# Performance work log

Measured on AMD Instinct MI355X. Metric: run time of the kernel, lower is better.

Reference implementation:

```python
import math
import jax, jax.numpy as jnp
import numpy as np

H = 32          # query heads
KV = 8          # key/value heads (GQA)
D = 128         # head_dim
PAGE = 16       # Quest page size
TOPK = 256      # page budget
THETA = 10000.0


def _rope(x, pos):
    # x: [..., D]; llama rotate_half RoPE at scalar position pos
    half = D // 2
    inv = 1.0 / (THETA ** (jnp.arange(half, dtype=jnp.float32) * 2.0 / D))
    ang = pos * inv                                   # [half]
    cos = jnp.concatenate([jnp.cos(ang), jnp.cos(ang)])  # [D]
    sin = jnp.concatenate([jnp.sin(ang), jnp.sin(ang)])
    rot = jnp.concatenate([-x[..., half:], x[..., :half]], axis=-1)
    return x * cos + rot * sin


def setup_inputs() -> dict:
    key = jax.random.key(0)
    ks = jax.random.split(key, 7)
    hid = H * D
    s = 1.0 / math.sqrt(hid)
    return {
        "hidden_states": jax.random.normal(ks[0], (1, 1, hid), jnp.float32),
        "k_cache": jax.random.normal(ks[1], (32767, KV, D), jnp.float32),
        "v_cache": jax.random.normal(ks[2], (32767, KV, D), jnp.float32),
        "Wq": jax.random.normal(ks[3], (hid, H * D), jnp.float32) * s,
        "Wk": jax.random.normal(ks[4], (hid, KV * D), jnp.float32) * s,
        "Wv": jax.random.normal(ks[5], (hid, KV * D), jnp.float32) * s,
        "Wo": jax.random.normal(ks[6], (H * D, hid), jnp.float32) * s,
    }


def reference(hidden_states, k_cache, v_cache, Wq, Wk, Wv, Wo):
    x = hidden_states[0]                    # [1, hidden]
    q = (x @ Wq).reshape(H, D)              # decode: q_len == 1
    k = (x @ Wk).reshape(KV, D)
    v = (x @ Wv).reshape(KV, D)

    past = k_cache.shape[0]
    q = _rope(q, jnp.float32(past))
    k = _rope(k, jnp.float32(past))

    # append_kv: paged cache, seqlen = past + 1 = n_pages * PAGE
    Kc = jnp.concatenate([k_cache, k[None]], axis=0)   # [S, KV, D]
    Vc = jnp.concatenate([v_cache, v[None]], axis=0)
    S = past + 1
    n_pages = S // PAGE

    # decode_estimate: per-page min/max key metadata, Quest upper-bound score
    Kp = Kc.reshape(n_pages, PAGE, KV, D)
    kmax = Kp.max(axis=1)                   # [P, KV, D]
    kmin = Kp.min(axis=1)
    G = H // KV
    qh = q.reshape(KV, G, D)
    pmax = qh[None] * kmax[:, :, None, :]   # [P, KV, G, D]
    pmin = qh[None] * kmin[:, :, None, :]
    score = jnp.maximum(pmax, pmin).sum(-1) # [P, KV, G]
    score = score.reshape(n_pages, H).T     # [H, P]
    # most recent page always attended
    score = score.at[:, -1].set(jnp.inf)

    # decode_topk: per-head page selection
    _, pidx = jax.lax.top_k(score, TOPK)    # [H, TOPK]
    tok = (pidx[..., None] * PAGE + jnp.arange(PAGE)).reshape(H, -1)  # [H, T]

    # decode_sparse_attn: gather selected pages (GQA mapping) + attention
    kvmap = jnp.arange(H) // G              # query head -> kv head
    Ksel = Kc[tok, kvmap[:, None]]          # [H, T, D]
    Vsel = Vc[tok, kvmap[:, None]]
    att = jnp.einsum('hd,htd->ht', q, Ksel) * (1.0 / math.sqrt(D))
    w = jax.nn.softmax(att, axis=-1)
    out = jnp.einsum('ht,htd->hd', w, Vsel) # [H, D]

    y = out.reshape(1, H * D) @ Wo          # o_proj
    return y[None]                          # [1, 1, hidden]
```

## Files before the change

### kernel.cpp

```cpp
#include <hip/hip_runtime.h>
#include <math.h>

#define H 32
#define KV 8
#define D 128
#define PAGE 16
#define TOPK 256
#define NPAGES 2048
#define PAST 32767
#define HID 4096

#define WS_Q      0
#define WS_K      4096
#define WS_V      5120
#define WS_SCORES 6144
#define WS_PIDX   71680
#define WS_PART_M 79872
#define WS_PART_L 80896
#define WS_PART_O 81920
#define WS_ATTN   212992

#define NCHUNK 32
#define PPC    8

__global__ void qkv_kernel(const float* __restrict__ x,
                           const float* __restrict__ Wq,
                           const float* __restrict__ Wk,
                           const float* __restrict__ Wv,
                           float* __restrict__ ws) {
    __shared__ float xs[64];
    int tid = threadIdx.x;
    int rc = blockIdx.x / 6;
    int cg = blockIdx.x % 6;
    int r0 = rc * 64;
    if (tid < 64) xs[tid] = x[r0 + tid];
    __syncthreads();
    const float* W; int Cc; int col; float* dst;
    if (cg < 4)       { W = Wq; Cc = 4096; col = cg * 1024 + tid * 4; dst = ws + WS_Q + col; }
    else if (cg == 4) { W = Wk; Cc = 1024; col = tid * 4;             dst = ws + WS_K + col; }
    else              { W = Wv; Cc = 1024; col = tid * 4;             dst = ws + WS_V + col; }
    const float* Wp = W + (size_t)r0 * Cc + col;
    float4 acc = {0.f, 0.f, 0.f, 0.f};
#pragma unroll 8
    for (int r = 0; r < 64; ++r) {
        float4 w4 = *(const float4*)(Wp + (size_t)r * Cc);
        float xr = xs[r];
        acc.x = fmaf(xr, w4.x, acc.x);
        acc.y = fmaf(xr, w4.y, acc.y);
        acc.z = fmaf(xr, w4.z, acc.z);
        acc.w = fmaf(xr, w4.w, acc.w);
    }
    atomicAdd(dst + 0, acc.x);
    atomicAdd(dst + 1, acc.y);
    atomicAdd(dst + 2, acc.z);
    atomicAdd(dst + 3, acc.w);
}

__global__ void rope_kernel(float* __restrict__ ws) {
    int idx = blockIdx.x * blockDim.x + threadIdx.x;
    if (idx >= 2560) return;
    float* base;
    if (idx < 2048) base = ws + WS_Q + (idx >> 6) * 128;
    else            base = ws + WS_K + ((idx - 2048) >> 6) * 128;
    int j = idx & 63;
    double t = (double)j / 64.0;
    float p = (float)pow(10000.0, t);
    float invf = 1.0f / p;
    float ang = 32767.0f * invf;
    float c = (float)cos((double)ang);
    float s = (float)sin((double)ang);
    float x0 = base[j], x1 = base[j + 64];
    base[j]      = x0 * c - x1 * s;
    base[j + 64] = x1 * c + x0 * s;
}

__global__ void score_kernel(const float* __restrict__ kc,
                             const float* __restrict__ q,
                             float* __restrict__ scores) {
    int tid = threadIdx.x;
    int lane = tid & 63;
    int wv = tid >> 6;
    int sub = lane & 31;
    int hf = lane >> 5;
    int p = blockIdx.x >> 1;
    int kv = ((blockIdx.x & 1) << 2) + wv;
    const float* kp0 = kc + ((size_t)(p * PAGE) * KV + kv) * D + 4 * sub;
    float4 mx = {-INFINITY, -INFINITY, -INFINITY, -INFINITY};
    float4 mn = { INFINITY,  INFINITY,  INFINITY,  INFINITY};
#pragma unroll
    for (int s8 = 0; s8 < 8; ++s8) {
        int t = 2 * s8 + hf;
        float4 v = *(const float4*)(kp0 + (size_t)t * (KV * D));
        mx.x = fmaxf(mx.x, v.x); mn.x = fminf(mn.x, v.x);
        mx.y = fmaxf(mx.y, v.y); mn.y = fminf(mn.y, v.y);
        mx.z = fmaxf(mx.z, v.z); mn.z = fminf(mn.z, v.z);
        mx.w = fmaxf(mx.w, v.w); mn.w = fminf(mn.w, v.w);
    }
    mx.x = fmaxf(mx.x, __shfl_xor(mx.x, 32)); mn.x = fminf(mn.x, __shfl_xor(mn.x, 32));
    mx.y = fmaxf(mx.y, __shfl_xor(mx.y, 32)); mn.y = fminf(mn.y, __shfl_xor(mn.y, 32));
    mx.z = fmaxf(mx.z, __shfl_xor(mx.z, 32)); mn.z = fminf(mn.z, __shfl_xor(mn.z, 32));
    mx.w = fmaxf(mx.w, __shfl_xor(mx.w, 32)); mn.w = fminf(mn.w, __shfl_xor(mn.w, 32));
    float sacc[4];
#pragma unroll
    for (int g = 0; g < 4; ++g) {
        float4 qq = *(const float4*)(q + (size_t)(kv * 4 + g) * 128 + 4 * sub);
        sacc[g] = fmaxf(qq.x * mx.x, qq.x * mn.x) + fmaxf(qq.y * mx.y, qq.y * mn.y)
                + fmaxf(qq.z * mx.z, qq.z * mn.z) + fmaxf(qq.w * mx.w, qq.w * mn.w);
    }
#pragma unroll
    for (int off = 16; off > 0; off >>= 1) {
#pragma unroll
        for (int g = 0; g < 4; ++g) sacc[g] += __shfl_xor(sacc[g], off);
    }
    if (lane == 0) {
#pragma unroll
        for (int g = 0; g < 4; ++g)
            scores[(size_t)(kv * 4 + g) * NPAGES + p] = sacc[g];
    }
}

__global__ void topk_kernel(const float* __restrict__ scores, int* __restrict__ pidx) {
    __shared__ unsigned su[NPAGES];
    __shared__ int hist[256];
    __shared__ int scan[256];
    __shared__ int wtot[4];
    __shared__ int cnt;
    __shared__ unsigned s_prefix;
    __shared__ int s_k;
    int tid = threadIdx.x;
    int lane = tid & 63;
    int wv = tid >> 6;
    int h = blockIdx.x;
    for (int i = tid; i < NPAGES; i += 256) {
        unsigned u;
        if (i == NPAGES - 1) u = 0xFFFFFFFFu;
        else {
            int b = __float_as_int(scores[(size_t)h * NPAGES + i]);
            u = (b >= 0) ? ((unsigned)b | 0x80000000u) : ~(unsigned)b;
        }
        su[i] = u;
    }
    if (tid == 0) cnt = 0;
    __syncthreads();

    unsigned prefix = 0;
    int K = TOPK;
    for (int level = 3; level >= 0; --level) {
        int shift = level * 8;
        unsigned pmask = (level == 3) ? 0u : (0xFFFFFFFFu << (shift + 8));
        hist[tid] = 0;
        __syncthreads();
        for (int i = tid; i < NPAGES; i += 256) {
            unsigned u = su[i];
            if ((u & pmask) == prefix)
                atomicAdd(&hist[(u >> shift) & 0xFF], 1);
        }
        __syncthreads();
        int v = hist[tid];
#pragma unroll
        for (int off = 1; off < 64; off <<= 1) {
            int o = __shfl_down(v, off);
            if (lane + off < 64) v += o;
        }
        if (lane == 0) wtot[wv] = v;
        __syncthreads();
        int add = 0;
        for (int w2 = wv + 1; w2 < 4; ++w2) add += wtot[w2];
        v += add;
        scan[tid] = v;
        __syncthreads();
        int nxt = (tid < 255) ? scan[tid + 1] : 0;
        if (v >= K && nxt < K) {
            s_prefix = prefix | ((unsigned)tid << shift);
            s_k = K - nxt;
        }
        __syncthreads();
        prefix = s_prefix;
        K = s_k;
        __syncthreads();
    }
    unsigned T = prefix;

    for (int i = tid; i < NPAGES; i += 256) {
        if (su[i] > T) {
            int pos = atomicAdd(&cnt, 1);
            pidx[h * TOPK + pos] = i;
        }
    }
    int base = TOPK - K;
    int i0 = tid * (NPAGES / 256);
    int tcount = 0;
#pragma unroll
    for (int j = 0; j < NPAGES / 256; ++j) if (su[i0 + j] == T) ++tcount;
    int sc = tcount;
#pragma unroll
    for (int off = 1; off < 64; off <<= 1) {
        int o = __shfl_up(sc, off);
        if (lane >= off) sc += o;
    }
    __syncthreads();
    if (lane == 63) wtot[wv] = sc;
    __syncthreads();
    int wadd = 0;
    for (int w2 = 0; w2 < wv; ++w2) wadd += wtot[w2];
    int pos = base + (sc - tcount) + wadd;
#pragma unroll
    for (int j = 0; j < NPAGES / 256; ++j) {
        if (su[i0 + j] == T) {
            if (pos < TOPK) pidx[h * TOPK + pos] = i0 + j;
            ++pos;
        }
    }
}

__global__ void attn_kernel(const float* __restrict__ kc,
                            const float* __restrict__ vc,
                            const float* __restrict__ ws,
                            const int* __restrict__ pidx,
                            float* __restrict__ part_m,
                            float* __restrict__ part_l,
                            float* __restrict__ part_o) {
    int tid = threadIdx.x;
    int lane = tid & 63;
    int wv = tid >> 6;
    int sub = lane & 31;
    int hf = lane >> 5;
    int h = blockIdx.x >> 5;
    int c = blockIdx.x & 31;
    int kvh = h >> 2;
    __shared__ float qs[128];
    __shared__ float sm[8], sl[8];
    __shared__ float so[8 * 128];
    if (tid < 128) qs[tid] = ws[WS_Q + h * 128 + tid];
    __syncthreads();
    float4 q4 = *(const float4*)(qs + 4 * sub);
    int hidx = wv * 2 + hf;
    int page = pidx[h * TOPK + c * PPC + hidx];
    size_t base = ((size_t)(page * PAGE) * KV + kvh) * D + 4 * sub;
    bool last = (page == NPAGES - 1);
    const float scale = 0.08838834764831843f;

    float s[PAGE];
#pragma unroll
    for (int t = 0; t < PAGE; ++t) {
        const float* kp = (last && t == PAGE - 1) ? (ws + WS_K + kvh * 128 + 4 * sub)
                                                  : (kc + base + (size_t)t * (KV * D));
        float4 kk = *(const float4*)kp;
        float d = q4.x * kk.x + q4.y * kk.y + q4.z * kk.z + q4.w * kk.w;
#pragma unroll
        for (int off = 16; off > 0; off >>= 1) d += __shfl_xor(d, off);
        s[t] = d * scale;
    }
    float m = -INFINITY;
#pragma unroll
    for (int t = 0; t < PAGE; ++t) m = fmaxf(m, s[t]);
    float l = 0.f;
    float4 o = {0.f, 0.f, 0.f, 0.f};
#pragma unroll
    for (int t = 0; t < PAGE; ++t) {
        float w = expf(s[t] - m);
        l += w;
        const float* vp = (last && t == PAGE - 1) ? (ws + WS_V + kvh * 128 + 4 * sub)
                                                  : (vc + base + (size_t)t * (KV * D));
        float4 vv = *(const float4*)vp;
        o.x = fmaf(w, vv.x, o.x);
        o.y = fmaf(w, vv.y, o.y);
        o.z = fmaf(w, vv.z, o.z);
        o.w = fmaf(w, vv.w, o.w);
    }
    if (sub == 0) { sm[hidx] = m; sl[hidx] = l; }
    *(float4*)(so + hidx * 128 + 4 * sub) = o;
    __syncthreads();
    if (tid < 128) {
        float M = -INFINITY;
#pragma unroll
        for (int w2 = 0; w2 < 8; ++w2) M = fmaxf(M, sm[w2]);
        float L = 0.f, O = 0.f;
#pragma unroll
        for (int w2 = 0; w2 < 8; ++w2) {
            float f = expf(sm[w2] - M);
            L += f * sl[w2];
            O += f * so[w2 * 128 + tid];
        }
        int pc = h * NCHUNK + c;
        if (tid == 0) { part_m[pc] = M; part_l[pc] = L; }
        part_o[(size_t)pc * 128 + tid] = O;
    }
}

__global__ void combine_kernel(const float* __restrict__ part_m,
                               const float* __restrict__ part_l,
                               const float* __restrict__ part_o,
                               float* __restrict__ attn) {
    int h = blockIdx.x;
    int d = threadIdx.x;
    float M = -INFINITY;
    for (int c = 0; c < NCHUNK; ++c) M = fmaxf(M, part_m[h * NCHUNK + c]);
    float L = 0.f, O = 0.f;
    for (int c = 0; c < NCHUNK; ++c) {
        float f = expf(part_m[h * NCHUNK + c] - M);
        L += f * part_l[h * NCHUNK + c];
        O += f * part_o[(size_t)(h * NCHUNK + c) * 128 + d];
    }
    attn[h * 128 + d] = O / L;
}

__global__ void wo_kernel(const float* __restrict__ attn,
                          const float* __restrict__ Wo,
                          float* __restrict__ out) {
    __shared__ float xs[64];
    int tid = threadIdx.x;
    int rc = blockIdx.x >> 2;
    int cb = blockIdx.x & 3;
    int r0 = rc * 64;
    if (tid < 64) xs[tid] = attn[r0 + tid];
    __syncthreads();
    int col = cb * 1024 + tid * 4;
    const float* Wp = Wo + (size_t)r0 * 4096 + col;
    float4 acc = {0.f, 0.f, 0.f, 0.f};
#pragma unroll 8
    for (int r = 0; r < 64; ++r) {
        float4 w4 = *(const float4*)(Wp + (size_t)r * 4096);
        float xr = xs[r];
        acc.x = fmaf(xr, w4.x, acc.x);
        acc.y = fmaf(xr, w4.y, acc.y);
        acc.z = fmaf(xr, w4.z, acc.z);
        acc.w = fmaf(xr, w4.w, acc.w);
    }
    atomicAdd(out + col + 0, acc.x);
    atomicAdd(out + col + 1, acc.y);
    atomicAdd(out + col + 2, acc.z);
    atomicAdd(out + col + 3, acc.w);
}

extern "C" void kernel_launch(void* const* d_in, const int* in_sizes, int n_in,
                              void* d_out, int out_size, void* d_ws, size_t ws_size,
                              hipStream_t stream) {
    const float* x  = (const float*)d_in[0];
    const float* kc = (const float*)d_in[1];
    const float* vc = (const float*)d_in[2];
    const float* Wq = (const float*)d_in[3];
    const float* Wk = (const float*)d_in[4];
    const float* Wv = (const float*)d_in[5];
    const float* Wo = (const float*)d_in[6];
    float* ws = (float*)d_ws;
    float* out = (float*)d_out;

    hipMemsetAsync(ws, 0, 6144 * sizeof(float), stream);
    hipMemsetAsync(out, 0, (size_t)out_size * sizeof(float), stream);

    qkv_kernel<<<384, 256, 0, stream>>>(x, Wq, Wk, Wv, ws);
    rope_kernel<<<10, 256, 0, stream>>>(ws);
    score_kernel<<<(NPAGES - 1) * 2, 256, 0, stream>>>(kc, ws + WS_Q, ws + WS_SCORES);
    topk_kernel<<<H, 256, 0, stream>>>(ws + WS_SCORES, (int*)(ws + WS_PIDX));
    attn_kernel<<<H * NCHUNK, 256, 0, stream>>>(kc, vc, ws, (const int*)(ws + WS_PIDX),
                                                ws + WS_PART_M, ws + WS_PART_L, ws + WS_PART_O);
    combine_kernel<<<H, 128, 0, stream>>>(ws + WS_PART_M, ws + WS_PART_L, ws + WS_PART_O,
                                          ws + WS_ATTN);
    wo_kernel<<<256, 256, 0, stream>>>(ws + WS_ATTN, Wo, out);
}
```

Before: 402.7 us.

## Replace atomic GEMV reductions with partial buffers and fuse combine and RoPE stages

The QKV and output-projection GEMVs now write per-row-chunk partial sums to workspace instead of using float atomics, and separate reduction kernels sum them. RoPE is folded into the QKV reduction, and the attention-chunk combine is folded into the Wo GEMV prologue. The two memsets are dropped, and attention exponentials use the fast __expf intrinsic. This removes atomic contention and several launches, at the cost of extra workspace traffic, redundant combine work per Wo block, and slightly lower exp precision.

```diff
diff --git a/kernel.cpp b/kernel.cpp
--- a/kernel.cpp
+++ b/kernel.cpp
@@ -10,24 +10,25 @@
 #define PAST 32767
 #define HID 4096
 
-#define WS_Q      0
-#define WS_K      4096
-#define WS_V      5120
-#define WS_SCORES 6144
-#define WS_PIDX   71680
-#define WS_PART_M 79872
-#define WS_PART_L 80896
-#define WS_PART_O 81920
-#define WS_ATTN   212992
+#define WS_Q       0
+#define WS_K       4096
+#define WS_V       5120
+#define WS_SCORES  6144
+#define WS_PIDX    71680
+#define WS_PART_M  79872
+#define WS_PART_L  80896
+#define WS_PART_O  81920
+#define WS_QKVPART 212992
+#define WS_WOPART  606208
 
 #define NCHUNK 32
 #define PPC    8
 
-__global__ void qkv_kernel(const float* __restrict__ x,
-                           const float* __restrict__ Wq,
-                           const float* __restrict__ Wk,
-                           const float* __restrict__ Wv,
-                           float* __restrict__ ws) {
+__global__ void qkv1_kernel(const float* __restrict__ x,
+                            const float* __restrict__ Wq,
+                            const float* __restrict__ Wk,
+                            const float* __restrict__ Wv,
+                            float* __restrict__ part) {
     __shared__ float xs[64];
     int tid = threadIdx.x;
     int rc = blockIdx.x / 6;
@@ -35,10 +36,10 @@
     int r0 = rc * 64;
     if (tid < 64) xs[tid] = x[r0 + tid];
     __syncthreads();
-    const float* W; int Cc; int col; float* dst;
-    if (cg < 4)       { W = Wq; Cc = 4096; col = cg * 1024 + tid * 4; dst = ws + WS_Q + col; }
-    else if (cg == 4) { W = Wk; Cc = 1024; col = tid * 4;             dst = ws + WS_K + col; }
-    else              { W = Wv; Cc = 1024; col = tid * 4;             dst = ws + WS_V + col; }
+    const float* W; int Cc; int col; int gcol;
+    if (cg < 4)       { W = Wq; Cc = 4096; col = cg * 1024 + tid * 4; gcol = col; }
+    else if (cg == 4) { W = Wk; Cc = 1024; col = tid * 4;             gcol = 4096 + col; }
+    else              { W = Wv; Cc = 1024; col = tid * 4;             gcol = 5120 + col; }
     const float* Wp = W + (size_t)r0 * Cc + col;
     float4 acc = {0.f, 0.f, 0.f, 0.f};
 #pragma unroll 8
@@ -50,28 +51,35 @@
         acc.z = fmaf(xr, w4.z, acc.z);
         acc.w = fmaf(xr, w4.w, acc.w);
     }
-    atomicAdd(dst + 0, acc.x);
-    atomicAdd(dst + 1, acc.y);
-    atomicAdd(dst + 2, acc.z);
-    atomicAdd(dst + 3, acc.w);
-}
-
-__global__ void rope_kernel(float* __restrict__ ws) {
-    int idx = blockIdx.x * blockDim.x + threadIdx.x;
-    if (idx >= 2560) return;
-    float* base;
-    if (idx < 2048) base = ws + WS_Q + (idx >> 6) * 128;
-    else            base = ws + WS_K + ((idx - 2048) >> 6) * 128;
-    int j = idx & 63;
-    double t = (double)j / 64.0;
-    float p = (float)pow(10000.0, t);
-    float invf = 1.0f / p;
-    float ang = 32767.0f * invf;
-    float c = (float)cos((double)ang);
-    float s = (float)sin((double)ang);
-    float x0 = base[j], x1 = base[j + 64];
-    base[j]      = x0 * c - x1 * s;
-    base[j + 64] = x1 * c + x0 * s;
+    *(float4*)(part + (size_t)rc * 6144 + gcol) = acc;
+}
+
+__global__ void reduce_rope_kernel(const float* __restrict__ part,
+                                   float* __restrict__ qkv) {
+    __shared__ float smem[256];
+    int tid = threadIdx.x;
+    int c = blockIdx.x * 256 + tid;
+    float s = 0.f;
+#pragma unroll 8
+    for (int rc = 0; rc < 64; ++rc) s += part[(size_t)rc * 6144 + c];
+    smem[tid] = s;
+    __syncthreads();
+    float outv;
+    if (c < 5120) {
+        int j = c & 127;
+        int jj = (j < 64) ? j : (j - 64);
+        double t = (double)jj / 64.0;
+        float p = (float)pow(10000.0, t);
+        float invf = 1.0f / p;
+        float ang = 32767.0f * invf;
+        float co = (float)cos((double)ang);
+        float si = (float)sin((double)ang);
+        if (j < 64) { float x0 = s, x1 = smem[tid + 64]; outv = x0 * co - x1 * si; }
+        else        { float x1 = s, x0 = smem[tid - 64]; outv = x1 * co + x0 * si; }
+    } else {
+        outv = s;
+    }
+    qkv[c] = outv;
 }
 
 __global__ void score_kernel(const float* __restrict__ kc,
@@ -258,7 +266,7 @@
     float4 o = {0.f, 0.f, 0.f, 0.f};
 #pragma unroll
     for (int t = 0; t < PAGE; ++t) {
-        float w = expf(s[t] - m);
+        float w = __expf(s[t] - m);
         l += w;
         const float* vp = (last && t == PAGE - 1) ? (ws + WS_V + kvh * 128 + 4 * sub)
                                                   : (vc + base + (size_t)t * (KV * D));
@@ -278,7 +286,7 @@
         float L = 0.f, O = 0.f;
 #pragma unroll
         for (int w2 = 0; w2 < 8; ++w2) {
-            float f = expf(sm[w2] - M);
+            float f = __expf(sm[w2] - M);
             L += f * sl[w2];
             O += f * so[w2 * 128 + tid];
         }
@@ -288,32 +296,32 @@
     }
 }
 
-__global__ void combine_kernel(const float* __restrict__ part_m,
-                               const float* __restrict__ part_l,
-                               const float* __restrict__ part_o,
-                               float* __restrict__ attn) {
-    int h = blockIdx.x;
-    int d = threadIdx.x;
-    float M = -INFINITY;
-    for (int c = 0; c < NCHUNK; ++c) M = fmaxf(M, part_m[h * NCHUNK + c]);
-    float L = 0.f, O = 0.f;
-    for (int c = 0; c < NCHUNK; ++c) {
-        float f = expf(part_m[h * NCHUNK + c] - M);
-        L += f * part_l[h * NCHUNK + c];
-        O += f * part_o[(size_t)(h * NCHUNK + c) * 128 + d];
-    }
-    attn[h * 128 + d] = O / L;
-}
-
-__global__ void wo_kernel(const float* __restrict__ attn,
-                          const float* __restrict__ Wo,
-                          float* __restrict__ out) {
+__global__ void wo1_kernel(const float* __restrict__ part_m,
+                           const float* __restrict__ part_l,
+                           const float* __restrict__ part_o,
+                           const float* __restrict__ Wo,
+                           float* __restrict__ wpart) {
     __shared__ float xs[64];
     int tid = threadIdx.x;
     int rc = blockIdx.x >> 2;
     int cb = blockIdx.x & 3;
     int r0 = rc * 64;
-    if (tid < 64) xs[tid] = attn[r0 + tid];
+    int h0 = r0 >> 7;
+    int dbase = r0 & 127;
+    if (tid < 64) {
+        int d = dbase + tid;
+        float M = -INFINITY;
+#pragma unroll
+        for (int c = 0; c < NCHUNK; ++c) M = fmaxf(M, part_m[h0 * NCHUNK + c]);
+        float L = 0.f, O = 0.f;
+#pragma unroll
+        for (int c = 0; c < NCHUNK; ++c) {
+            float f = __expf(part_m[h0 * NCHUNK + c] - M);
+            L += f * part_l[h0 * NCHUNK + c];
+            O += f * part_o[(size_t)(h0 * NCHUNK + c) * 128 + d];
+        }
+        xs[tid] = O / L;
+    }
     __syncthreads();
     int col = cb * 1024 + tid * 4;
     const float* Wp = Wo + (size_t)r0 * 4096 + col;
@@ -327,10 +335,20 @@
         acc.z = fmaf(xr, w4.z, acc.z);
         acc.w = fmaf(xr, w4.w, acc.w);
     }
-    atomicAdd(out + col + 0, acc.x);
-    atomicAdd(out + col + 1, acc.y);
-    atomicAdd(out + col + 2, acc.z);
-    atomicAdd(out + col + 3, acc.w);
+    *(float4*)(wpart + (size_t)rc * 4096 + col) = acc;
+}
+
+__global__ void wo2_kernel(const float* __restrict__ wpart,
+                           float* __restrict__ out) {
+    int tid = threadIdx.x;
+    int col = blockIdx.x * 1024 + tid * 4;
+    float4 acc = {0.f, 0.f, 0.f, 0.f};
+#pragma unroll 8
+    for (int rc = 0; rc < 64; ++rc) {
+        float4 p = *(const float4*)(wpart + (size_t)rc * 4096 + col);
+        acc.x += p.x; acc.y += p.y; acc.z += p.z; acc.w += p.w;
+    }
+    *(float4*)(out + col) = acc;
 }
 
 extern "C" void kernel_launch(void* const* d_in, const int* in_sizes, int n_in,
@@ -346,16 +364,13 @@
     float* ws = (float*)d_ws;
     float* out = (float*)d_out;
 
-    hipMemsetAsync(ws, 0, 6144 * sizeof(float), stream);
-    hipMemsetAsync(out, 0, (size_t)out_size * sizeof(float), stream);
-
-    qkv_kernel<<<384, 256, 0, stream>>>(x, Wq, Wk, Wv, ws);
-    rope_kernel<<<10, 256, 0, stream>>>(ws);
+    qkv1_kernel<<<384, 256, 0, stream>>>(x, Wq, Wk, Wv, ws + WS_QKVPART);
+    reduce_rope_kernel<<<24, 256, 0, stream>>>(ws + WS_QKVPART, ws + WS_Q);
     score_kernel<<<(NPAGES - 1) * 2, 256, 0, stream>>>(kc, ws + WS_Q, ws + WS_SCORES);
     topk_kernel<<<H, 256, 0, stream>>>(ws + WS_SCORES, (int*)(ws + WS_PIDX));
     attn_kernel<<<H * NCHUNK, 256, 0, stream>>>(kc, vc, ws, (const int*)(ws + WS_PIDX),
                                                 ws + WS_PART_M, ws + WS_PART_L, ws + WS_PART_O);
-    combine_kernel<<<H, 128, 0, stream>>>(ws + WS_PART_M, ws + WS_PART_L, ws + WS_PART_O,
-                                          ws + WS_ATTN);
-    wo_kernel<<<256, 256, 0, stream>>>(ws + WS_ATTN, Wo, out);
-}
+    wo1_kernel<<<256, 256, 0, stream>>>(ws + WS_PART_M, ws + WS_PART_L, ws + WS_PART_O,
+                                        Wo, ws + WS_WOPART);
+    wo2_kernel<<<4, 256, 0, stream>>>(ws + WS_WOPART, out);
+}
```

Result: no change. 400.7 us (-0.5%).
